# Optimization experiments

Measured on AMD Instinct MI355X. Metric: run time of the kernel, lower is better.

The kernel has to match this reference:

```python
import jax, jax.numpy as jnp
import numpy as np

N_TASKS = 8
D_MODEL = 1024
HIDDEN = 1024
N_CLASSES = 100
BATCH = 8192


def setup_inputs() -> dict:
    key = jax.random.key(0)
    ks = jax.random.split(key, 6)
    s1 = 1.0 / np.sqrt(D_MODEL)
    s2 = 1.0 / np.sqrt(HIDDEN)
    return {
        "x": jax.random.normal(ks[0], (BATCH, D_MODEL), dtype=jnp.float32),
        "task_id": jax.random.randint(ks[1], (BATCH,), 0, N_TASKS),
        "W1": jax.random.uniform(ks[2], (N_TASKS, D_MODEL, HIDDEN), jnp.float32, -s1, s1),
        "b1": jax.random.uniform(ks[3], (N_TASKS, HIDDEN), jnp.float32, -s1, s1),
        "W2": jax.random.uniform(ks[4], (N_TASKS, HIDDEN, N_CLASSES), jnp.float32, -s2, s2),
        "b2": jax.random.uniform(ks[5], (N_TASKS, N_CLASSES), jnp.float32, -s2, s2),
    }


def reference(x, task_id, W1, b1, W2, b2):
    # Per-task 2-layer MLP heads; dropout is identity (inference).
    # Compute all heads batched, then select each row's head via one-hot.
    h = jax.nn.relu(jnp.einsum("bd,tdh->tbh", x, W1) + b1[:, None, :])  # [T,B,H]
    logits = jnp.einsum("tbh,thc->tbc", h, W2) + b2[:, None, :]          # [T,B,C]
    onehot = jax.nn.one_hot(task_id, W1.shape[0], dtype=x.dtype)          # [B,T]
    return jnp.einsum("tbc,bt->bc", logits, onehot)                      # [B,C]
```

## Files before the change

kernel.cpp:

```cpp
#include <hip/hip_runtime.h>
#include <hip/hip_bf16.h>
#include <stdint.h>

#define T_TASKS 8
#define DM      1024
#define HID     1024
#define NC      100
#define NCP     128
#define BATCH   8192
#define MPAD    9216

typedef __bf16 bf16x8 __attribute__((ext_vector_type(8)));
typedef float  f32x4  __attribute__((ext_vector_type(4)));
typedef unsigned int u32;
#define GAS __attribute__((address_space(1)))
#define LAS __attribute__((address_space(3)))

__device__ __forceinline__ unsigned short f2bf(float f) {
  __hip_bfloat16 h = __float2bfloat16(f);
  return __builtin_bit_cast(unsigned short, h);
}

__device__ __forceinline__ float bf2f(unsigned short u) {
  const u32 v = ((u32)u) << 16;
  return __builtin_bit_cast(float, v);
}

__global__ void count_k(const int* __restrict__ task_id,
                        int* __restrict__ gcount, int* __restrict__ perm) {
  __shared__ int h[T_TASKS];
  const int tid = threadIdx.x;
  const int bx  = blockIdx.x;
  if (tid < T_TASKS) h[tid] = 0;
  __syncthreads();
  atomicAdd(&h[task_id[bx * 256 + tid]], 1);
  const int base = bx * (MPAD / 32);
  for (int i = tid; i < MPAD / 32; i += 256) perm[base + i] = -1;
  __syncthreads();
  if (tid < T_TASKS) gcount[bx * T_TASKS + tid] = h[tid];
}

__global__ void scatter_k(const int* __restrict__ task_id,
                          const int* __restrict__ gcount,
                          int* __restrict__ perm, int* __restrict__ starts) {
  __shared__ int h[T_TASKS];
  __shared__ int tot[T_TASKS], prev[T_TASKS];
  __shared__ int sst[T_TASKS + 1];
  const int tid = threadIdx.x;
  const int bx  = blockIdx.x;
  if (tid < T_TASKS) {
    h[tid] = 0;
    int s = 0, p = 0;
    for (int b = 0; b < 32; ++b) {
      const int c = gcount[b * T_TASKS + tid];
      s += c;
      if (b < bx) p += c;
    }
    tot[tid] = s; prev[tid] = p;
  }
  __syncthreads();
  if (tid == 0) {
    int off = 0;
    for (int t = 0; t < T_TASKS; ++t) { sst[t] = off; off += (tot[t] + 127) & ~127; }
    sst[T_TASKS] = off;
  }
  const int r = bx * 256 + tid;
  const int t = task_id[r];
  const int slot = atomicAdd(&h[t], 1);
  __syncthreads();
  perm[sst[t] + prev[t] + slot] = r;
  if (bx == 0 && tid <= T_TASKS) starts[tid] = sst[tid];
}

#define GX_BLKS MPAD
#define W1_BLKS (T_TASKS * 16 * 16)
#define W2_BLKS (16 * T_TASKS)
__global__ void preproc_fused(const float* __restrict__ x,
                              const int* __restrict__ perm,
                              unsigned short* __restrict__ XP,
                              const float* __restrict__ W1,
                              unsigned short* __restrict__ W1T,
                              const float* __restrict__ W2,
                              unsigned short* __restrict__ W2F) {
  __shared__ unsigned short tile[128 * 72];
  const int bid = blockIdx.x;
  const int tid = threadIdx.x;

  if (bid < GX_BLKS) {
    const int r = perm[bid];
    const int c = tid * 4;
    ushort4 v;
    if (r >= 0) {
      const float4 f = *(const float4*)(x + (size_t)r * DM + c);
      v.x = f2bf(f.x); v.y = f2bf(f.y); v.z = f2bf(f.z); v.w = f2bf(f.w);
    } else {
      v.x = 0; v.y = 0; v.z = 0; v.w = 0;
    }
    *(ushort4*)(XP + (size_t)bid * DM + c) = v;
    return;
  }

  if (bid < GX_BLKS + W1_BLKS) {
    const int b  = bid - GX_BLKS;
    const int t  = b >> 8;
    const int rem = b & 255;
    const int d0 = (rem >> 4) * 64;
    const int h0 = (rem & 15) * 64;
    const float* src = W1 + (size_t)t * DM * HID;
    unsigned short* dst = W1T + (size_t)t * HID * DM;
#pragma unroll
    for (int i = 0; i < 4; ++i) {
      const int idx = tid + 256 * i;
      const int d  = idx >> 4;
      const int hc = (idx & 15) * 4;
      const float4 f = *(const float4*)(src + (size_t)(d0 + d) * HID + h0 + hc);
      tile[(hc + 0) * 65 + d] = f2bf(f.x);
      tile[(hc + 1) * 65 + d] = f2bf(f.y);
      tile[(hc + 2) * 65 + d] = f2bf(f.z);
      tile[(hc + 3) * 65 + d] = f2bf(f.w);
    }
    __syncthreads();
#pragma unroll
    for (int i = 0; i < 2; ++i) {
      const int idx = tid + 256 * i;
      const int lh  = idx >> 3;
      const int ldc = idx & 7;
      union { uint4 v; unsigned short s[8]; } o;
#pragma unroll
      for (int q = 0; q < 8; ++q) o.s[q] = tile[lh * 65 + ldc * 8 + q];
      *(uint4*)(dst + (size_t)(h0 + lh) * DM + d0 + ldc * 8) = o.v;
    }
    return;
  }

  {
    const int b  = bid - (GX_BLKS + W1_BLKS);
    const int t  = b >> 4;
    const int h0 = (b & 15) * 64;
    const float* src = W2 + (size_t)t * HID * NC;
#pragma unroll
    for (int i = 0; i < 36; ++i) tile[tid + 256 * i] = 0;
    __syncthreads();
#pragma unroll
    for (int i = 0; i < 32; ++i) {
      const int idx = tid + 256 * i;
      const int row = idx >> 7, col = idx & 127;
      if (col < NC)
        tile[col * 72 + row] = f2bf(src[(size_t)(h0 + row) * NC + col]);
    }
    __syncthreads();
    const int w = tid >> 6, lane = tid & 63;
    const int lr = lane & 15, quad = lane >> 4;
#pragma unroll
    for (int e = 0; e < 4; ++e) {
      const int fi = w * 4 + e;
      const int ci = fi >> 1, kcl = fi & 1;
      const uint4 v = *(const uint4*)&tile[(ci * 16 + lr) * 72 + kcl * 32 + quad * 8];
      unsigned short* dstp =
          W2F + (((size_t)t * 8 + ci) * 32 + (h0 >> 5) + kcl) * 512 + lane * 8;
      *(uint4*)dstp = v;
    }
  }
}

__global__ __launch_bounds__(256, 3) void gemm_fused4(
    const unsigned short* __restrict__ XP,
    const unsigned short* __restrict__ W1T,
    const unsigned short* __restrict__ W2F,
    const float* __restrict__ b1,
    const int* __restrict__ starts,
    unsigned short* __restrict__ Lp)
{
  __shared__ __align__(16) unsigned short lds[18432];
  unsigned short* As = lds;
  unsigned short* Bs = lds + 8192;
  unsigned short* hS = lds;

  const int tid = threadIdx.x;
  const int p0  = blockIdx.x * 128;
  const int n0  = blockIdx.y * 128;

  if (p0 >= starts[T_TASKS]) return;

  int task = 0;
#pragma unroll
  for (int t = 1; t < T_TASKS; ++t)
    if (p0 >= starts[t]) task = t;

  const int wave = tid >> 6;
  const int lane = tid & 63;
  const int wm   = (wave >> 1) * 64;
  const int wn   = (wave & 1) * 64;
  const int lr   = lane & 15;
  const int quad = lane >> 4;

  const int crow = tid >> 3;
  const int kc   = (tid & 7) ^ (crow & 7);
  const unsigned short* pA[4];
  const unsigned short* pB[4];
  const unsigned short* Bg = W1T + ((size_t)task * HID + n0) * 1024;
#pragma unroll
  for (int i = 0; i < 4; ++i) {
    const int row = crow + 32 * i;
    pA[i] = XP + (size_t)(p0 + row) * 1024 + kc * 8;
    pB[i] = Bg + (size_t)row * 1024 + kc * 8;
  }

  f32x4 acc[4][4];
#pragma unroll
  for (int i = 0; i < 4; ++i)
#pragma unroll
    for (int j = 0; j < 4; ++j) acc[i][j] = (f32x4){0.f, 0.f, 0.f, 0.f};

  const int sw0 = quad ^ (lr & 7);
  const int sw1 = (4 + quad) ^ (lr & 7);

  for (int k0 = 0; k0 < 1024; k0 += 64) {
#pragma unroll
    for (int i = 0; i < 4; ++i) {
      __builtin_amdgcn_global_load_lds((const GAS u32*)(pA[i] + k0),
                                       (LAS u32*)&As[(tid + 256 * i) * 8], 16, 0, 0);
      __builtin_amdgcn_global_load_lds((const GAS u32*)(pB[i] + k0),
                                       (LAS u32*)&Bs[(tid + 256 * i) * 8], 16, 0, 0);
    }
    __syncthreads();
    {
      bf16x8 a[4], b[4];
#pragma unroll
      for (int i = 0; i < 4; ++i)
        a[i] = *(const bf16x8*)&As[((wm + i * 16 + lr) * 8 + sw0) * 8];
#pragma unroll
      for (int j = 0; j < 4; ++j)
        b[j] = *(const bf16x8*)&Bs[((wn + j * 16 + lr) * 8 + sw0) * 8];
#pragma unroll
      for (int i = 0; i < 4; ++i)
#pragma unroll
        for (int j = 0; j < 4; ++j)
          acc[i][j] = __builtin_amdgcn_mfma_f32_16x16x32_bf16(a[i], b[j], acc[i][j], 0, 0, 0);
#pragma unroll
      for (int i = 0; i < 4; ++i)
        a[i] = *(const bf16x8*)&As[((wm + i * 16 + lr) * 8 + sw1) * 8];
#pragma unroll
      for (int j = 0; j < 4; ++j)
        b[j] = *(const bf16x8*)&Bs[((wn + j * 16 + lr) * 8 + sw1) * 8];
#pragma unroll
      for (int i = 0; i < 4; ++i)
#pragma unroll
        for (int j = 0; j < 4; ++j)
          acc[i][j] = __builtin_amdgcn_mfma_f32_16x16x32_bf16(a[i], b[j], acc[i][j], 0, 0, 0);
    }
    __syncthreads();
  }

  float b1v[4];
#pragma unroll
  for (int ni = 0; ni < 4; ++ni)
    b1v[ni] = b1[task * HID + n0 + wn + ni * 16 + lr];
#pragma unroll
  for (int mi = 0; mi < 4; ++mi)
#pragma unroll
    for (int r = 0; r < 4; ++r) {
      const int row = wm + mi * 16 + quad * 4 + r;
#pragma unroll
      for (int ni = 0; ni < 4; ++ni) {
        float v = acc[mi][ni][r] + b1v[ni];
        v = v > 0.f ? v : 0.f;
        hS[row * 136 + wn + ni * 16 + lr] = f2bf(v);
      }
    }
  __syncthreads();

  const int cbase = (wave & 1) * 4;
  const unsigned short* pW2 =
      W2F + (((size_t)task * 8 + cbase) * 32 + blockIdx.y * 4) * 512 + lane * 8;

  f32x4 acc2[4][4];
#pragma unroll
  for (int mi = 0; mi < 4; ++mi)
#pragma unroll
    for (int ci = 0; ci < 4; ++ci) acc2[mi][ci] = (f32x4){0.f, 0.f, 0.f, 0.f};

#pragma unroll
  for (int e = 0; e < 4; ++e) {
    bf16x8 w2p[4], a2[4];
#pragma unroll
    for (int ci = 0; ci < 4; ++ci)
      w2p[ci] = *(const bf16x8*)(pW2 + ((size_t)ci * 32 + e) * 512);
#pragma unroll
    for (int mi = 0; mi < 4; ++mi)
      a2[mi] = *(const bf16x8*)&hS[(wm + mi * 16 + lr) * 136 + e * 32 + quad * 8];
#pragma unroll
    for (int mi = 0; mi < 4; ++mi)
#pragma unroll
      for (int ci = 0; ci < 4; ++ci)
        acc2[mi][ci] = __builtin_amdgcn_mfma_f32_16x16x32_bf16(
            a2[mi], w2p[ci], acc2[mi][ci], 0, 0, 0);
  }

  unsigned short* lp = Lp + ((size_t)blockIdx.y * MPAD + p0) * NCP;
#pragma unroll
  for (int mi = 0; mi < 4; ++mi)
#pragma unroll
    for (int r = 0; r < 4; ++r) {
      const int row = wm + mi * 16 + quad * 4 + r;
#pragma unroll
      for (int ci = 0; ci < 4; ++ci)
        lp[row * NCP + wn + ci * 16 + lr] = f2bf(acc2[mi][ci][r]);
    }
}

__global__ void reduce_k(const unsigned short* __restrict__ Lp,
                         const int* __restrict__ perm,
                         const int* __restrict__ task_id,
                         const float* __restrict__ b2,
                         float* __restrict__ Out) {
  const int gid = blockIdx.x * 256 + threadIdx.x;
  const int row = gid >> 5;
  const int c4  = (gid & 31) * 4;
  if (c4 >= NC) return;
  const int og = perm[row];
  if (og < 0) return;
  float s0 = 0.f, s1 = 0.f, s2 = 0.f, s3 = 0.f;
#pragma unroll
  for (int sp = 0; sp < 8; ++sp) {
    const ushort4 v = *(const ushort4*)(Lp + ((size_t)sp * MPAD + row) * NCP + c4);
    s0 += bf2f(v.x); s1 += bf2f(v.y); s2 += bf2f(v.z); s3 += bf2f(v.w);
  }
  const int task = task_id[og];
  const float4 bb = *(const float4*)(b2 + (size_t)task * NC + c4);
  float4 o;
  o.x = s0 + bb.x; o.y = s1 + bb.y; o.z = s2 + bb.z; o.w = s3 + bb.w;
  *(float4*)(Out + (size_t)og * NC + c4) = o;
}

extern "C" void kernel_launch(void* const* d_in, const int* in_sizes, int n_in,
                              void* d_out, int out_size, void* d_ws, size_t ws_size,
                              hipStream_t stream) {
  const float* x       = (const float*)d_in[0];
  const int*   task_id = (const int*)d_in[1];
  const float* W1      = (const float*)d_in[2];
  const float* b1      = (const float*)d_in[3];
  const float* W2      = (const float*)d_in[4];
  const float* b2      = (const float*)d_in[5];
  float* out = (float*)d_out;

  char* ws = (char*)d_ws;
  int* perm   = (int*)(ws + 0);
  int* gcount = (int*)(ws + 36864);
  int* starts = (int*)(ws + 37888);
  unsigned short* XP  = (unsigned short*)(ws + 65536);
  unsigned short* W1T = (unsigned short*)(ws + 18939904);
  unsigned short* W2F = (unsigned short*)(ws + 35717120);
  unsigned short* Lp  = (unsigned short*)(ws + 37814272);

  count_k<<<32, 256, 0, stream>>>(task_id, gcount, perm);
  scatter_k<<<32, 256, 0, stream>>>(task_id, gcount, perm, starts);
  preproc_fused<<<GX_BLKS + W1_BLKS + W2_BLKS, 256, 0, stream>>>(
      x, perm, XP, W1, W1T, W2, W2F);
  gemm_fused4<<<dim3(MPAD / 128, HID / 128), 256, 0, stream>>>(
      XP, W1T, W2F, b1, starts, Lp);
  reduce_k<<<MPAD * 32 / 256, 256, 0, stream>>>(Lp, perm, task_id, b2, out);
}
```

Baseline: 151.9 us.

## Merge sort kernels with weight preprocessing and remap GEMM blocks per XCD

Replaces the separate count and scatter kernels with one redundant per-block histogram inside the weight-conversion kernel, so the sort runs alongside the W1/W2 transposes. The row gather moves into its own kernel that launches after the sort. Only the padding slots of perm are now set to -1, since every real slot is written by the scatter. Separately, GEMM block indices are remapped so consecutive row tiles land on the same XCD, which should improve L2 reuse of weight tiles. The trade-off is that every sort block recomputes the full histogram on its own.

```diff
diff --git a/kernel.cpp b/kernel.cpp
--- a/kernel.cpp
+++ b/kernel.cpp
@@ -26,82 +26,75 @@
   return __builtin_bit_cast(float, v);
 }
 
-__global__ void count_k(const int* __restrict__ task_id,
-                        int* __restrict__ gcount, int* __restrict__ perm) {
-  __shared__ int h[T_TASKS];
-  const int tid = threadIdx.x;
-  const int bx  = blockIdx.x;
-  if (tid < T_TASKS) h[tid] = 0;
-  __syncthreads();
-  atomicAdd(&h[task_id[bx * 256 + tid]], 1);
-  const int base = bx * (MPAD / 32);
-  for (int i = tid; i < MPAD / 32; i += 256) perm[base + i] = -1;
-  __syncthreads();
-  if (tid < T_TASKS) gcount[bx * T_TASKS + tid] = h[tid];
-}
-
-__global__ void scatter_k(const int* __restrict__ task_id,
-                          const int* __restrict__ gcount,
-                          int* __restrict__ perm, int* __restrict__ starts) {
-  __shared__ int h[T_TASKS];
-  __shared__ int tot[T_TASKS], prev[T_TASKS];
-  __shared__ int sst[T_TASKS + 1];
-  const int tid = threadIdx.x;
-  const int bx  = blockIdx.x;
-  if (tid < T_TASKS) {
-    h[tid] = 0;
-    int s = 0, p = 0;
-    for (int b = 0; b < 32; ++b) {
-      const int c = gcount[b * T_TASKS + tid];
-      s += c;
-      if (b < bx) p += c;
-    }
-    tot[tid] = s; prev[tid] = p;
-  }
-  __syncthreads();
-  if (tid == 0) {
-    int off = 0;
-    for (int t = 0; t < T_TASKS; ++t) { sst[t] = off; off += (tot[t] + 127) & ~127; }
-    sst[T_TASKS] = off;
-  }
-  const int r = bx * 256 + tid;
-  const int t = task_id[r];
-  const int slot = atomicAdd(&h[t], 1);
-  __syncthreads();
-  perm[sst[t] + prev[t] + slot] = r;
-  if (bx == 0 && tid <= T_TASKS) starts[tid] = sst[tid];
-}
-
-#define GX_BLKS MPAD
+#define SORT_BLKS 32
 #define W1_BLKS (T_TASKS * 16 * 16)
 #define W2_BLKS (16 * T_TASKS)
-__global__ void preproc_fused(const float* __restrict__ x,
-                              const int* __restrict__ perm,
-                              unsigned short* __restrict__ XP,
-                              const float* __restrict__ W1,
-                              unsigned short* __restrict__ W1T,
-                              const float* __restrict__ W2,
-                              unsigned short* __restrict__ W2F) {
-  __shared__ unsigned short tile[128 * 72];
+__global__ void sortpre_k(const int* __restrict__ task_id,
+                          const float* __restrict__ W1,
+                          unsigned short* __restrict__ W1T,
+                          const float* __restrict__ W2,
+                          unsigned short* __restrict__ W2F,
+                          int* __restrict__ perm, int* __restrict__ starts) {
+  __shared__ __align__(16) unsigned short tile[128 * 72];
+  __shared__ int sAux[25];
   const int bid = blockIdx.x;
   const int tid = threadIdx.x;
 
-  if (bid < GX_BLKS) {
-    const int r = perm[bid];
-    const int c = tid * 4;
-    ushort4 v;
-    if (r >= 0) {
-      const float4 f = *(const float4*)(x + (size_t)r * DM + c);
-      v.x = f2bf(f.x); v.y = f2bf(f.y); v.z = f2bf(f.z); v.w = f2bf(f.w);
-    } else {
-      v.x = 0; v.y = 0; v.z = 0; v.w = 0;
-    }
-    *(ushort4*)(XP + (size_t)bid * DM + c) = v;
+  if (bid < SORT_BLKS) {
+    int* hist = (int*)tile;
+    int* tot  = sAux;
+    int* prev = sAux + 8;
+    int* sst  = sAux + 16;
+#pragma unroll
+    for (int t = 0; t < T_TASKS; ++t) hist[tid * 8 + t] = 0;
+    __syncthreads();
+    const int cbase = tid * 32;
+    for (int i = 0; i < 32; ++i) {
+      const int t = task_id[cbase + i];
+      hist[tid * 8 + t] += 1;
+    }
+    __syncthreads();
+    if (tid < T_TASKS) {
+      int s = 0;
+      for (int r = 0; r < 256; ++r) s += hist[r * 8 + tid];
+      tot[tid] = s;
+    } else if (tid < 2 * T_TASKS) {
+      const int t = tid - T_TASKS;
+      const int lim = bid * 8;
+      int s = 0;
+      for (int r = 0; r < lim; ++r) s += hist[r * 8 + t];
+      prev[t] = s;
+    }
+    __syncthreads();
+    if (tid == 0) {
+      int off = 0;
+      for (int t = 0; t < T_TASKS; ++t) { sst[t] = off; off += (tot[t] + 127) & ~127; }
+      sst[T_TASKS] = off;
+    }
+    if (tid < T_TASKS) hist[tid] = 0;
+    __syncthreads();
+    const int r = bid * 256 + tid;
+    const int t = task_id[r];
+    const int slot = atomicAdd(&hist[t], 1);
+    perm[sst[t] + prev[t] + slot] = r;
+    if (tid < 32) {
+      const int g = bid * 32 + tid;
+      int acc = 0, pos = -1;
+#pragma unroll
+      for (int t2 = 0; t2 < T_TASKS; ++t2) {
+        const int pc = sst[t2 + 1] - sst[t2] - tot[t2];
+        if (pos < 0 && g < acc + pc) pos = sst[t2] + tot[t2] + (g - acc);
+        acc += pc;
+      }
+      if (pos < 0) pos = sst[T_TASKS] + (g - acc);
+      perm[pos] = -1;
+    }
+    if (bid == 0 && tid <= T_TASKS) starts[tid] = sst[tid];
     return;
   }
 
-  if (bid < GX_BLKS + W1_BLKS) {
-    const int b  = bid - GX_BLKS;
+  if (bid < SORT_BLKS + W1_BLKS) {
+    const int b  = bid - SORT_BLKS;
     const int t  = b >> 8;
     const int rem = b & 255;
     const int d0 = (rem >> 4) * 64;
@@ -134,7 +127,7 @@
   }
 
   {
-    const int b  = bid - (GX_BLKS + W1_BLKS);
+    const int b  = bid - (SORT_BLKS + W1_BLKS);
     const int t  = b >> 4;
     const int h0 = (b & 15) * 64;
     const float* src = W2 + (size_t)t * HID * NC;
@@ -161,6 +154,23 @@
       *(uint4*)dstp = v;
     }
   }
+}
+
+__global__ void gather_k(const float* __restrict__ x,
+                         const int* __restrict__ perm,
+                         unsigned short* __restrict__ XP) {
+  const int bid = blockIdx.x;
+  const int tid = threadIdx.x;
+  const int r = perm[bid];
+  const int c = tid * 4;
+  ushort4 v;
+  if (r >= 0) {
+    const float4 f = *(const float4*)(x + (size_t)r * DM + c);
+    v.x = f2bf(f.x); v.y = f2bf(f.y); v.z = f2bf(f.z); v.w = f2bf(f.w);
+  } else {
+    v.x = 0; v.y = 0; v.z = 0; v.w = 0;
+  }
+  *(ushort4*)(XP + (size_t)bid * DM + c) = v;
 }
 
 __global__ __launch_bounds__(256, 3) void gemm_fused4(
@@ -177,8 +187,15 @@
   unsigned short* hS = lds;
 
   const int tid = threadIdx.x;
-  const int p0  = blockIdx.x * 128;
-  const int n0  = blockIdx.y * 128;
+
+  const int L   = blockIdx.y * gridDim.x + blockIdx.x;
+  const int xcd = L & 7;
+  const int idx = L >> 3;
+  const int bx  = xcd * 9 + (idx % 9);
+  const int by  = idx / 9;
+
+  const int p0  = bx * 128;
+  const int n0  = by * 128;
 
   if (p0 >= starts[T_TASKS]) return;
 
@@ -272,7 +289,7 @@
 
   const int cbase = (wave & 1) * 4;
   const unsigned short* pW2 =
-      W2F + (((size_t)task * 8 + cbase) * 32 + blockIdx.y * 4) * 512 + lane * 8;
+      W2F + (((size_t)task * 8 + cbase) * 32 + by * 4) * 512 + lane * 8;
 
   f32x4 acc2[4][4];
 #pragma unroll
@@ -297,7 +314,7 @@
             a2[mi], w2p[ci], acc2[mi][ci], 0, 0, 0);
   }
 
-  unsigned short* lp = Lp + ((size_t)blockIdx.y * MPAD + p0) * NCP;
+  unsigned short* lp = Lp + ((size_t)by * MPAD + p0) * NCP;
 #pragma unroll
   for (int mi = 0; mi < 4; ++mi)
 #pragma unroll
@@ -346,17 +363,15 @@
 
   char* ws = (char*)d_ws;
   int* perm   = (int*)(ws + 0);
-  int* gcount = (int*)(ws + 36864);
   int* starts = (int*)(ws + 37888);
   unsigned short* XP  = (unsigned short*)(ws + 65536);
   unsigned short* W1T = (unsigned short*)(ws + 18939904);
   unsigned short* W2F = (unsigned short*)(ws + 35717120);
   unsigned short* Lp  = (unsigned short*)(ws + 37814272);
 
-  count_k<<<32, 256, 0, stream>>>(task_id, gcount, perm);
-  scatter_k<<<32, 256, 0, stream>>>(task_id, gcount, perm, starts);
-  preproc_fused<<<GX_BLKS + W1_BLKS + W2_BLKS, 256, 0, stream>>>(
-      x, perm, XP, W1, W1T, W2, W2F);
+  sortpre_k<<<SORT_BLKS + W1_BLKS + W2_BLKS, 256, 0, stream>>>(
+      task_id, W1, W1T, W2, W2F, perm, starts);
+  gather_k<<<MPAD, 256, 0, stream>>>(x, perm, XP);
   gemm_fused4<<<dim3(MPAD / 128, HID / 128), 256, 0, stream>>>(
       XP, W1T, W2F, b1, starts, Lp);
   reduce_k<<<MPAD * 32 / 256, 256, 0, stream>>>(Lp, perm, task_id, b2, out);
```

Result: no change. 149.4 us (-1.6%).
